# Optimization experiments

Hardware: AMD Instinct MI355X
Metric: run time of the kernel (lower is better)

## Reference

```python
import jax, jax.numpy as jnp
import numpy as np

N_SRC = 50000
N_DST = 50000
E = 1600000
IN_DIM = 128
OUT_DIM = 128
EDGE_DIM = 64
NUM_HEADS = 4
HEAD_DIM = OUT_DIM // NUM_HEADS


def setup_inputs() -> dict:
    key = jax.random.key(0)
    ks = jax.random.split(key, 10)
    return {
        "h_src": jax.random.normal(ks[0], (N_SRC, IN_DIM), dtype=jnp.float32),
        "h_dst": jax.random.normal(ks[1], (N_DST, IN_DIM), dtype=jnp.float32),
        "edge_feat": jax.random.normal(ks[2], (E, EDGE_DIM), dtype=jnp.float32),
        "edge_index": jnp.stack([
            jax.random.randint(ks[3], (E,), 0, N_SRC),
            jax.random.randint(ks[4], (E,), 0, N_DST),
        ], axis=0).astype(jnp.int64) if False else jnp.stack([
            jax.random.randint(ks[3], (E,), 0, N_SRC),
            jax.random.randint(ks[4], (E,), 0, N_DST),
        ], axis=0),
        # weights stored [in, out]; y = x @ W (same math as torch Linear with W^T)
        "W_src": jax.random.normal(ks[5], (IN_DIM, OUT_DIM), dtype=jnp.float32) * 0.05,
        "W_dst": jax.random.normal(ks[6], (IN_DIM, OUT_DIM), dtype=jnp.float32) * 0.05,
        "W_edge": jax.random.normal(ks[7], (EDGE_DIM, OUT_DIM), dtype=jnp.float32) * 0.05,
        "a_src": jax.random.normal(ks[8], (NUM_HEADS, HEAD_DIM), dtype=jnp.float32) * 0.1,
        "a_dst": jax.random.normal(ks[9], (NUM_HEADS, HEAD_DIM), dtype=jnp.float32) * 0.1,
        "a_edge": jax.random.normal(jax.random.fold_in(key, 10), (NUM_HEADS, HEAD_DIM), dtype=jnp.float32) * 0.1,
    }


def reference(h_src, h_dst, edge_feat, edge_index, W_src, W_dst, W_edge, a_src, a_dst, a_edge):
    num_dst = h_dst.shape[0]
    src_idx, dst_idx = edge_index[0], edge_index[1]

    hs = (h_src @ W_src).reshape(-1, NUM_HEADS, HEAD_DIM)   # [N_src, H, D]
    hd = (h_dst @ W_dst).reshape(-1, NUM_HEADS, HEAD_DIM)   # [N_dst, H, D]
    he = (edge_feat @ W_edge).reshape(-1, NUM_HEADS, HEAD_DIM)  # [E, H, D]

    # per-node attention logit components, gathered to edges
    e_src_n = jnp.einsum('nhd,hd->nh', hs, a_src)  # [N_src, H]
    e_dst_n = jnp.einsum('nhd,hd->nh', hd, a_dst)  # [N_dst, H]
    e_edge = jnp.einsum('ehd,hd->eh', he, a_edge)  # [E, H]
    e = e_src_n[src_idx] + e_dst_n[dst_idx] + e_edge  # [E, H]
    e = jnp.where(e > 0, e, 0.2 * e)  # leaky_relu(0.2)

    # segmented softmax over edges grouped by destination node
    e_max = jax.ops.segment_max(e, dst_idx, num_segments=num_dst)  # [N_dst, H]
    e_max = jnp.where(jnp.isfinite(e_max), e_max, 0.0)  # empty segments
    e_exp = jnp.exp(e - e_max[dst_idx])  # [E, H]
    e_sum = jax.ops.segment_sum(e_exp, dst_idx, num_segments=num_dst)  # [N_dst, H]
    alpha = e_exp / (e_sum[dst_idx] + 1e-8)  # [E, H]

    # weighted scatter-aggregate of source features
    msg = alpha[..., None] * hs[src_idx]  # [E, H, D]
    out = jax.ops.segment_sum(msg, dst_idx, num_segments=num_dst)  # [N_dst, H, D]
    return out.reshape(num_dst, NUM_HEADS * HEAD_DIM)
```

## Files before the change

### kernel.cpp

```cpp
#include <hip/hip_runtime.h>

typedef _Float16 half_t;

#define N_SRCN 50000
#define N_DSTN 50000
#define NE     1600000
#define IN_DIM 128
#define OUT_DIMN 128
#define EDGE_DIMN 64
#define NHEAD  4
#define HDIM   32

#define ROR_ADD(x, CTRL) ((x) + __int_as_float(__builtin_amdgcn_update_dpp( \
    0, __float_as_int(x), (CTRL), 0xF, 0xF, false)))
__device__ __forceinline__ float sum16(float s) {
    s = ROR_ADD(s, 0x121);
    s = ROR_ADD(s, 0x122);
    s = ROR_ADD(s, 0x124);
    s = ROR_ADD(s, 0x128);
    return s;
}


__global__ __launch_bounds__(512) void k_combine(
    const float* __restrict__ Wsrc, const float* __restrict__ Wdst,
    const float* __restrict__ Wedge,
    const float* __restrict__ asrc, const float* __restrict__ adst,
    const float* __restrict__ aedge,
    float* __restrict__ c_srcH, float* __restrict__ c_dstH,
    float* __restrict__ c_edgeH) {
    int t = threadIdx.x;
    int k = t >> 2, h = t & 3;
    float s1 = 0.f, s2 = 0.f;
    #pragma unroll
    for (int d = 0; d < HDIM; ++d) {
        s1 += Wsrc[k * OUT_DIMN + h * HDIM + d] * asrc[h * HDIM + d];
        s2 += Wdst[k * OUT_DIMN + h * HDIM + d] * adst[h * HDIM + d];
    }
    c_srcH[h * IN_DIM + k] = s1;
    c_dstH[h * IN_DIM + k] = s2;
    if (t < EDGE_DIMN * NHEAD) {
        float s3 = 0.f;
        #pragma unroll
        for (int d = 0; d < HDIM; ++d)
            s3 += Wedge[k * OUT_DIMN + h * HDIM + d] * aedge[h * HDIM + d];
        c_edgeH[h * EDGE_DIMN + k] = s3;
    }
}

__global__ __launch_bounds__(256) void k_node_logits(
    const float* __restrict__ X, const float* __restrict__ cH,
    float* __restrict__ outl, int N) {
    int t = threadIdx.x;
    int row = blockIdx.x * 16 + (t >> 4);
    int q = t & 15;
    if (row >= N) return;
    const float4* X4 = (const float4*)X;
    const float4* C4 = (const float4*)cH;
    float4 xa = X4[(size_t)row * 32 + q];
    float4 xb = X4[(size_t)row * 32 + 16 + q];
    float s0, s1, s2, s3;
    #pragma unroll
    for (int h = 0; h < 4; ++h) {
        float4 ca = C4[h * 32 + q];
        float4 cb = C4[h * 32 + 16 + q];
        float v = xa.x * ca.x + xa.y * ca.y + xa.z * ca.z + xa.w * ca.w
                + xb.x * cb.x + xb.y * cb.y + xb.z * cb.z + xb.w * cb.w;
        v = sum16(v);
        if (h == 0) s0 = v; else if (h == 1) s1 = v;
        else if (h == 2) s2 = v; else s3 = v;
    }
    float v = (q == 0) ? s0 : (q == 1) ? s1 : (q == 2) ? s2 : s3;
    if (q < 4) outl[(size_t)row * 4 + q] = v;
}

__global__ __launch_bounds__(256) void k_hist(
    const int* __restrict__ dstI, int* __restrict__ counts) {
    int e = blockIdx.x * 256 + threadIdx.x;
    if (e < NE) atomicAdd(&counts[dstI[e]], 1);
}

__global__ __launch_bounds__(1024) void k_scan_part(
    const int* __restrict__ cnt, int* __restrict__ offs, int* __restrict__ bsum) {
    __shared__ int wsum[16];
    int t = threadIdx.x, b = blockIdx.x;
    int idx = b * 1024 + t;
    int lane = t & 63, w = t >> 6;
    int c = (idx < N_DSTN) ? cnt[idx] : 0;
    int incl = c;
    #pragma unroll
    for (int off = 1; off < 64; off <<= 1) {
        int v = __shfl_up(incl, off, 64);
        if (lane >= off) incl += v;
    }
    if (lane == 63) wsum[w] = incl;
    __syncthreads();
    if (t == 0) {
        int run = 0;
        #pragma unroll
        for (int qq = 0; qq < 16; ++qq) { int v = wsum[qq]; wsum[qq] = run; run += v; }
        bsum[b] = run;
    }
    __syncthreads();
    if (idx < N_DSTN) offs[idx] = wsum[w] + incl - c;
}

__global__ __launch_bounds__(64) void k_scan_mid(
    int* __restrict__ bsum, int* __restrict__ offs, int nb) {
    int l = threadIdx.x;
    int v = (l < nb) ? bsum[l] : 0;
    int incl = v;
    #pragma unroll
    for (int off = 1; off < 64; off <<= 1) {
        int u = __shfl_up(incl, off, 64);
        if (l >= off) incl += u;
    }
    if (l < nb) bsum[l] = incl - v;
    if (l == 63) offs[N_DSTN] = incl;
}

__global__ __launch_bounds__(1024) void k_scan_add(
    int* __restrict__ offs, int* __restrict__ cursor, const int* __restrict__ bsum) {
    int idx = blockIdx.x * 1024 + threadIdx.x;
    if (idx < N_DSTN) {
        int v = offs[idx] + bsum[blockIdx.x];
        offs[idx] = v;
        cursor[idx] = v;
    }
}

__global__ __launch_bounds__(256) void k_scatter(
    const int* __restrict__ dstI, int* __restrict__ cursor,
    int* __restrict__ perm) {
    int e = blockIdx.x * 256 + threadIdx.x;
    if (e < NE) {
        int d = dstI[e];
        int pos = atomicAdd(&cursor[d], 1);
        perm[pos] = e;
    }
}

__global__ __launch_bounds__(256) void k_gemm_half(
    const float* __restrict__ A, const float* __restrict__ W,
    half_t* __restrict__ C, int M, int c0) {
    __shared__ float As[64][68];
    __shared__ float Ws[64][68];
    int t = threadIdx.x;
    int tx = t & 15, ty = t >> 4;
    int rowbase = blockIdx.x * 64;
    float acc[4][4];
    #pragma unroll
    for (int i = 0; i < 4; ++i)
        #pragma unroll
        for (int j = 0; j < 4; ++j) acc[i][j] = 0.f;

    for (int kc = 0; kc < IN_DIM; kc += 64) {
        #pragma unroll
        for (int p = 0; p < 4; ++p) {
            int flat = p * 1024 + t * 4;
            int r = flat >> 6, ck = flat & 63;
            float4 v = make_float4(0.f, 0.f, 0.f, 0.f);
            if (rowbase + r < M)
                v = *(const float4*)(A + (size_t)(rowbase + r) * IN_DIM + kc + ck);
            *(float4*)(&As[r][ck]) = v;
        }
        #pragma unroll
        for (int p = 0; p < 4; ++p) {
            int flat = p * 1024 + t * 4;
            int kk = flat >> 6, col = flat & 63;
            *(float4*)(&Ws[kk][col]) =
                *(const float4*)(W + (size_t)(kc + kk) * OUT_DIMN + c0 + col);
        }
        __syncthreads();
        #pragma unroll
        for (int k = 0; k < 64; ++k) {
            float a[4], b[4];
            #pragma unroll
            for (int i = 0; i < 4; ++i) a[i] = As[ty * 4 + i][k];
            #pragma unroll
            for (int j = 0; j < 4; ++j) b[j] = Ws[k][tx + j * 16];
            #pragma unroll
            for (int i = 0; i < 4; ++i)
                #pragma unroll
                for (int j = 0; j < 4; ++j) acc[i][j] += a[i] * b[j];
        }
        __syncthreads();
    }
    #pragma unroll
    for (int i = 0; i < 4; ++i) {
        int row = rowbase + ty * 4 + i;
        if (row < M) {
            #pragma unroll
            for (int j = 0; j < 4; ++j)
                C[(size_t)row * 64 + tx + j * 16] = (half_t)acc[i][j];
        }
    }
}

__global__ __launch_bounds__(256) void k_gather(
    const int* __restrict__ offs, const int* __restrict__ perm,
    const int* __restrict__ srcI,
    const float* __restrict__ EF, const float* __restrict__ ceH,
    const float* __restrict__ esrc, const float* __restrict__ edstl,
    const half_t* __restrict__ hsH, float* __restrict__ out, int pass) {
    int d = blockIdx.x * 4 + (threadIdx.x >> 6);
    if (d >= N_DSTN) return;
    int l = threadIdx.x & 63;
    int q = l & 15;
    int h = pass * 2 + (l >> 5);
    int start = offs[d], end = offs[d + 1];
    int n = end - start;
    if (n <= 0) { out[(size_t)d * OUT_DIMN + pass * 64 + l] = 0.f; return; }

    const float4* EF4 = (const float4*)EF;
    float4 c4 = ((const float4*)ceH)[h * 16 + q];
    float ed = edstl[(size_t)d * 4 + h];
    int end1 = end - 1;
    #define PCLAMP(i) perm[(start + (i) < end) ? (start + (i)) : end1]

    int a0 = PCLAMP(0), a1 = PCLAMP(1), a2 = PCLAMP(2);
    int e3 = PCLAMP(3), e4 = PCLAMP(4);
    int b0 = srcI[a0], b1 = srcI[a1], b2 = srcI[a2];
    int s3 = srcI[e3];
    float4 v0 = EF4[(size_t)a0 * 16 + q];
    float4 v1 = EF4[(size_t)a1 * 16 + q];
    float4 v2 = EF4[(size_t)a2 * 16 + q];
    float f0 = esrc[(size_t)b0 * 4 + h];
    float f1 = esrc[(size_t)b1 * 4 + h];
    float f2 = esrc[(size_t)b2 * 4 + h];
    half_t g0 = hsH[(size_t)b0 * 64 + l];
    half_t g1 = hsH[(size_t)b1 * 64 + l];
    half_t g2 = hsH[(size_t)b2 * 64 + l];

    float acc = 0.f, den = 0.f;
    for (int i = 0; i < n; ++i) {
        int e5 = PCLAMP(i + 5);
        int s4 = srcI[e4];
        float4 vN = EF4[(size_t)e3 * 16 + q];
        float  fN = esrc[(size_t)s3 * 4 + h];
        half_t gN = hsH[(size_t)s3 * 64 + l];

        float s = v0.x * c4.x + v0.y * c4.y + v0.z * c4.z + v0.w * c4.w;
        s = sum16(s);
        float z = f0 + ed + s;
        z = z > 0.f ? z : 0.2f * z;
        float ez = __expf(z);
        den += ez;
        acc += ez * (float)g0;

        v0 = v1; v1 = v2; v2 = vN;
        f0 = f1; f1 = f2; f2 = fN;
        g0 = g1; g1 = g2; g2 = gN;
        e3 = e4; e4 = e5; s3 = s4;
    }
    #undef PCLAMP
    out[(size_t)d * OUT_DIMN + pass * 64 + l] = acc / (den + 1e-8f);
}

extern "C" void kernel_launch(void* const* d_in, const int* in_sizes, int n_in,
                              void* d_out, int out_size, void* d_ws, size_t ws_size,
                              hipStream_t stream) {
    const float* h_src     = (const float*)d_in[0];
    const float* h_dst     = (const float*)d_in[1];
    const float* edge_feat = (const float*)d_in[2];
    const int*   eidx      = (const int*)d_in[3];
    const float* Wsrc      = (const float*)d_in[4];
    const float* Wdst      = (const float*)d_in[5];
    const float* Wedge     = (const float*)d_in[6];
    const float* asrc      = (const float*)d_in[7];
    const float* adst      = (const float*)d_in[8];
    const float* aedge     = (const float*)d_in[9];
    float* out = (float*)d_out;

    char* W = (char*)d_ws;
    half_t* hsH    = (half_t*)(W + 0);
    int*   perm    = (int*)(W + 6400000);
    float* esrc    = (float*)(W + 12800000);
    float* edstl   = (float*)(W + 13600000);
    int*   offs    = (int*)(W + 14400000);
    int*   cursor  = (int*)(W + 14600016);
    int*   counts  = (int*)(W + 14800016);
    float* c_srcH  = (float*)(W + 15000016);
    float* c_dstH  = (float*)(W + 15002064);
    float* c_edgeH = (float*)(W + 15004112);
    int*   bsum    = (int*)(W + 15005136);

    const int* srcI = eidx;
    const int* dstI = eidx + NE;

    const int NB_SCAN = (N_DSTN + 1023) / 1024;

    hipMemsetAsync(counts, 0, N_DSTN * sizeof(int), stream);

    k_combine<<<1, 512, 0, stream>>>(Wsrc, Wdst, Wedge, asrc, adst, aedge,
                                     c_srcH, c_dstH, c_edgeH);
    k_node_logits<<<(N_SRCN + 15) / 16, 256, 0, stream>>>(h_src, c_srcH, esrc, N_SRCN);
    k_node_logits<<<(N_DSTN + 15) / 16, 256, 0, stream>>>(h_dst, c_dstH, edstl, N_DSTN);

    k_hist<<<(NE + 255) / 256, 256, 0, stream>>>(dstI, counts);
    k_scan_part<<<NB_SCAN, 1024, 0, stream>>>(counts, offs, bsum);
    k_scan_mid<<<1, 64, 0, stream>>>(bsum, offs, NB_SCAN);
    k_scan_add<<<NB_SCAN, 1024, 0, stream>>>(offs, cursor, bsum);
    k_scatter<<<(NE + 255) / 256, 256, 0, stream>>>(dstI, cursor, perm);

    k_gemm_half<<<(N_SRCN + 63) / 64, 256, 0, stream>>>(h_src, Wsrc, hsH, N_SRCN, 0);
    k_gather<<<(N_DSTN + 3) / 4, 256, 0, stream>>>(offs, perm, srcI, edge_feat,
                                                   c_edgeH, esrc, edstl, hsH, out, 0);
    k_gemm_half<<<(N_SRCN + 63) / 64, 256, 0, stream>>>(h_src, Wsrc, hsH, N_SRCN, 64);
    k_gather<<<(N_DSTN + 3) / 4, 256, 0, stream>>>(offs, perm, srcI, edge_feat,
                                                   c_edgeH, esrc, edstl, hsH, out, 1);
}
```

Baseline: 1.405 ms.

## Stream edge logits in edge order and scatter compact CSR weights for gather

Edge-feature dot products and the exp'd leaky-relu logits are now computed in a coalesced pass over edges. That pass scatters 16-bit source indices and fp16 unnormalized weights into CSR order, replacing the perm-based random reads of 256-byte edge rows inside the gather. The gather now splits each head into four 32-column passes, with two half-waves each reducing half the edge list, and only reads compact per-edge arrays plus the source feature column. The cost is two edge-stream passes with atomics, four GEMM+gather passes instead of two, and fp16 storage of exp weights, which could overflow for large logits. It also relies on source ids fitting in 16 bits, which holds for 50000 nodes.

Result: faster. 1.216 ms (-13.4%).

```diff
diff --git a/kernel.cpp b/kernel.cpp
--- a/kernel.cpp
+++ b/kernel.cpp
@@ -120,37 +120,68 @@
 }
 
 __global__ __launch_bounds__(1024) void k_scan_add(
-    int* __restrict__ offs, int* __restrict__ cursor, const int* __restrict__ bsum) {
+    int* __restrict__ offs, int* __restrict__ curA, int* __restrict__ curB,
+    const int* __restrict__ bsum) {
     int idx = blockIdx.x * 1024 + threadIdx.x;
     if (idx < N_DSTN) {
         int v = offs[idx] + bsum[blockIdx.x];
         offs[idx] = v;
-        cursor[idx] = v;
-    }
-}
-
-__global__ __launch_bounds__(256) void k_scatter(
-    const int* __restrict__ dstI, int* __restrict__ cursor,
-    int* __restrict__ perm) {
-    int e = blockIdx.x * 256 + threadIdx.x;
-    if (e < NE) {
-        int d = dstI[e];
-        int pos = atomicAdd(&cursor[d], 1);
-        perm[pos] = e;
-    }
-}
-
-__global__ __launch_bounds__(256) void k_gemm_half(
+        curA[idx] = v;
+        curB[idx] = v;
+    }
+}
+
+__global__ __launch_bounds__(256) void k_edge_stream(
+    const float* __restrict__ EF,
+    const int* __restrict__ srcI, const int* __restrict__ dstI,
+    const float* __restrict__ esrc, const float* __restrict__ edstl,
+    const float* __restrict__ ceH, int* __restrict__ cursor,
+    unsigned short* __restrict__ ssrc,
+    half_t* __restrict__ wAo, half_t* __restrict__ wBo,
+    int ha, int hb) {
+    int t = threadIdx.x;
+    int e = blockIdx.x * 16 + (t >> 4);
+    if (e >= NE) return;
+    int q = t & 15;
+    const float4* EF4 = (const float4*)EF;
+    const float4* CE4 = (const float4*)ceH;
+    float4 v  = EF4[(size_t)e * 16 + q];
+    float4 cA = CE4[ha * 16 + q];
+    float4 cB = CE4[hb * 16 + q];
+    float sA = v.x * cA.x + v.y * cA.y + v.z * cA.z + v.w * cA.w;
+    float sB = v.x * cB.x + v.y * cB.y + v.z * cB.z + v.w * cB.w;
+    sA = sum16(sA);
+    sB = sum16(sB);
+    int pos = 0;
+    if (q < 2) {
+        int si = srcI[e], di = dstI[e];
+        int h = q ? hb : ha;
+        float s = q ? sB : sA;
+        float z = esrc[(size_t)si * 4 + h] + edstl[(size_t)di * 4 + h] + s;
+        z = z > 0.f ? z : 0.2f * z;
+        float ez = __expf(z);
+        if (q == 0) pos = atomicAdd(&cursor[di], 1);
+        pos = __shfl(pos, (t & 63) & ~15, 64);
+        if (q == 0) {
+            ssrc[pos] = (unsigned short)si;
+            wAo[pos] = (half_t)ez;
+        } else {
+            wBo[pos] = (half_t)ez;
+        }
+    }
+}
+
+__global__ __launch_bounds__(256) void k_gemm_q(
     const float* __restrict__ A, const float* __restrict__ W,
     half_t* __restrict__ C, int M, int c0) {
     __shared__ float As[64][68];
-    __shared__ float Ws[64][68];
+    __shared__ float Ws[64][36];
     int t = threadIdx.x;
-    int tx = t & 15, ty = t >> 4;
+    int tx = t & 7, ty = t >> 3;
     int rowbase = blockIdx.x * 64;
-    float acc[4][4];
-    #pragma unroll
-    for (int i = 0; i < 4; ++i)
+    float acc[2][4];
+    #pragma unroll
+    for (int i = 0; i < 2; ++i)
         #pragma unroll
         for (int j = 0; j < 4; ++j) acc[i][j] = 0.f;
 
@@ -165,96 +196,75 @@
             *(float4*)(&As[r][ck]) = v;
         }
         #pragma unroll
-        for (int p = 0; p < 4; ++p) {
+        for (int p = 0; p < 2; ++p) {
             int flat = p * 1024 + t * 4;
-            int kk = flat >> 6, col = flat & 63;
+            int kk = flat >> 5, col = flat & 31;
             *(float4*)(&Ws[kk][col]) =
                 *(const float4*)(W + (size_t)(kc + kk) * OUT_DIMN + c0 + col);
         }
         __syncthreads();
         #pragma unroll
         for (int k = 0; k < 64; ++k) {
-            float a[4], b[4];
+            float a[2], b[4];
             #pragma unroll
-            for (int i = 0; i < 4; ++i) a[i] = As[ty * 4 + i][k];
+            for (int i = 0; i < 2; ++i) a[i] = As[ty * 2 + i][k];
             #pragma unroll
-            for (int j = 0; j < 4; ++j) b[j] = Ws[k][tx + j * 16];
+            for (int j = 0; j < 4; ++j) b[j] = Ws[k][tx + j * 8];
             #pragma unroll
-            for (int i = 0; i < 4; ++i)
+            for (int i = 0; i < 2; ++i)
                 #pragma unroll
                 for (int j = 0; j < 4; ++j) acc[i][j] += a[i] * b[j];
         }
         __syncthreads();
     }
     #pragma unroll
-    for (int i = 0; i < 4; ++i) {
-        int row = rowbase + ty * 4 + i;
+    for (int i = 0; i < 2; ++i) {
+        int row = rowbase + ty * 2 + i;
         if (row < M) {
             #pragma unroll
             for (int j = 0; j < 4; ++j)
-                C[(size_t)row * 64 + tx + j * 16] = (half_t)acc[i][j];
+                C[(size_t)row * 32 + tx + j * 8] = (half_t)acc[i][j];
         }
     }
 }
 
 __global__ __launch_bounds__(256) void k_gather(
-    const int* __restrict__ offs, const int* __restrict__ perm,
-    const int* __restrict__ srcI,
-    const float* __restrict__ EF, const float* __restrict__ ceH,
-    const float* __restrict__ esrc, const float* __restrict__ edstl,
-    const half_t* __restrict__ hsH, float* __restrict__ out, int pass) {
+    const int* __restrict__ offs, const unsigned short* __restrict__ ssrc,
+    const half_t* __restrict__ wH, const half_t* __restrict__ hs_q,
+    float* __restrict__ out, int hcol) {
     int d = blockIdx.x * 4 + (threadIdx.x >> 6);
     if (d >= N_DSTN) return;
     int l = threadIdx.x & 63;
-    int q = l & 15;
-    int h = pass * 2 + (l >> 5);
+    int half = l >> 5, c = l & 31;
     int start = offs[d], end = offs[d + 1];
     int n = end - start;
-    if (n <= 0) { out[(size_t)d * OUT_DIMN + pass * 64 + l] = 0.f; return; }
-
-    const float4* EF4 = (const float4*)EF;
-    float4 c4 = ((const float4*)ceH)[h * 16 + q];
-    float ed = edstl[(size_t)d * 4 + h];
-    int end1 = end - 1;
-    #define PCLAMP(i) perm[(start + (i) < end) ? (start + (i)) : end1]
-
-    int a0 = PCLAMP(0), a1 = PCLAMP(1), a2 = PCLAMP(2);
-    int e3 = PCLAMP(3), e4 = PCLAMP(4);
-    int b0 = srcI[a0], b1 = srcI[a1], b2 = srcI[a2];
-    int s3 = srcI[e3];
-    float4 v0 = EF4[(size_t)a0 * 16 + q];
-    float4 v1 = EF4[(size_t)a1 * 16 + q];
-    float4 v2 = EF4[(size_t)a2 * 16 + q];
-    float f0 = esrc[(size_t)b0 * 4 + h];
-    float f1 = esrc[(size_t)b1 * 4 + h];
-    float f2 = esrc[(size_t)b2 * 4 + h];
-    half_t g0 = hsH[(size_t)b0 * 64 + l];
-    half_t g1 = hsH[(size_t)b1 * 64 + l];
-    half_t g2 = hsH[(size_t)b2 * 64 + l];
-
+    if (n <= 0) {
+        if (half == 0) out[(size_t)d * OUT_DIMN + hcol + c] = 0.f;
+        return;
+    }
+    int cntA = (n + 1) >> 1;
+    int myStart = start + (half ? cntA : 0);
+    int myN = half ? (n - cntA) : cntA;
+    int lim = (myN > 0) ? (myN - 1) : 0;
+    #define RIDX(j) (myStart + (((j) < lim) ? (j) : lim))
+
+    unsigned short s0 = ssrc[RIDX(0)], s1 = ssrc[RIDX(1)];
+    half_t w0 = wH[RIDX(0)], w1 = wH[RIDX(1)];
+    half_t h0 = hs_q[(size_t)s0 * 32 + c];
     float acc = 0.f, den = 0.f;
-    for (int i = 0; i < n; ++i) {
-        int e5 = PCLAMP(i + 5);
-        int s4 = srcI[e4];
-        float4 vN = EF4[(size_t)e3 * 16 + q];
-        float  fN = esrc[(size_t)s3 * 4 + h];
-        half_t gN = hsH[(size_t)s3 * 64 + l];
-
-        float s = v0.x * c4.x + v0.y * c4.y + v0.z * c4.z + v0.w * c4.w;
-        s = sum16(s);
-        float z = f0 + ed + s;
-        z = z > 0.f ? z : 0.2f * z;
-        float ez = __expf(z);
-        den += ez;
-        acc += ez * (float)g0;
-
-        v0 = v1; v1 = v2; v2 = vN;
-        f0 = f1; f1 = f2; f2 = fN;
-        g0 = g1; g1 = g2; g2 = gN;
-        e3 = e4; e4 = e5; s3 = s4;
-    }
-    #undef PCLAMP
-    out[(size_t)d * OUT_DIMN + pass * 64 + l] = acc / (den + 1e-8f);
+    for (int j = 0; j < cntA; ++j) {
+        unsigned short s2 = ssrc[RIDX(j + 2)];
+        half_t w2 = wH[RIDX(j + 2)];
+        half_t h1 = hs_q[(size_t)s1 * 32 + c];
+        float wf = (j < myN) ? (float)w0 : 0.f;
+        den += wf;
+        acc = fmaf(wf, (float)h0, acc);
+        s0 = s1; s1 = s2; w0 = w1; w1 = w2; h0 = h1;
+    }
+    #undef RIDX
+    acc += __shfl_xor(acc, 32, 64);
+    den += __shfl_xor(den, 32, 64);
+    if (half == 0) out[(size_t)d * OUT_DIMN + hcol + c] = acc / (den + 1e-8f);
 }
 
 extern "C" void kernel_launch(void* const* d_in, const int* in_sizes, int n_in,
@@ -273,17 +283,20 @@
     float* out = (float*)d_out;
 
     char* W = (char*)d_ws;
-    half_t* hsH    = (half_t*)(W + 0);
-    int*   perm    = (int*)(W + 6400000);
+    unsigned short* ssrc = (unsigned short*)(W + 0);
+    half_t* wA     = (half_t*)(W + 3200000);
+    half_t* wB     = (half_t*)(W + 6400000);
+    half_t* hs_q   = (half_t*)(W + 9600000);
     float* esrc    = (float*)(W + 12800000);
     float* edstl   = (float*)(W + 13600000);
     int*   offs    = (int*)(W + 14400000);
-    int*   cursor  = (int*)(W + 14600016);
-    int*   counts  = (int*)(W + 14800016);
-    float* c_srcH  = (float*)(W + 15000016);
-    float* c_dstH  = (float*)(W + 15002064);
-    float* c_edgeH = (float*)(W + 15004112);
-    int*   bsum    = (int*)(W + 15005136);
+    int*   curA    = (int*)(W + 14600016);
+    int*   curB    = (int*)(W + 14800016);
+    int*   counts  = (int*)(W + 15000016);
+    float* c_srcH  = (float*)(W + 15200016);
+    float* c_dstH  = (float*)(W + 15202064);
+    float* c_edgeH = (float*)(W + 15204112);
+    int*   bsum    = (int*)(W + 15205136);
 
     const int* srcI = eidx;
     const int* dstI = eidx + NE;
@@ -300,13 +313,19 @@
     k_hist<<<(NE + 255) / 256, 256, 0, stream>>>(dstI, counts);
     k_scan_part<<<NB_SCAN, 1024, 0, stream>>>(counts, offs, bsum);
     k_scan_mid<<<1, 64, 0, stream>>>(bsum, offs, NB_SCAN);
-    k_scan_add<<<NB_SCAN, 1024, 0, stream>>>(offs, cursor, bsum);
-    k_scatter<<<(NE + 255) / 256, 256, 0, stream>>>(dstI, cursor, perm);
-
-    k_gemm_half<<<(N_SRCN + 63) / 64, 256, 0, stream>>>(h_src, Wsrc, hsH, N_SRCN, 0);
-    k_gather<<<(N_DSTN + 3) / 4, 256, 0, stream>>>(offs, perm, srcI, edge_feat,
-                                                   c_edgeH, esrc, edstl, hsH, out, 0);
-    k_gemm_half<<<(N_SRCN + 63) / 64, 256, 0, stream>>>(h_src, Wsrc, hsH, N_SRCN, 64);
-    k_gather<<<(N_DSTN + 3) / 4, 256, 0, stream>>>(offs, perm, srcI, edge_feat,
-                                                   c_edgeH, esrc, edstl, hsH, out, 1);
-}
+    k_scan_add<<<NB_SCAN, 1024, 0, stream>>>(offs, curA, curB, bsum);
+
+    k_edge_stream<<<(NE + 15) / 16, 256, 0, stream>>>(
+        edge_feat, srcI, dstI, esrc, edstl, c_edgeH, curA, ssrc, wA, wB, 0, 1);
+    k_gemm_q<<<(N_SRCN + 63) / 64, 256, 0, stream>>>(h_src, Wsrc, hs_q, N_SRCN, 0);
+    k_gather<<<(N_DSTN + 3) / 4, 256, 0, stream>>>(offs, ssrc, wA, hs_q, out, 0);
+    k_gemm_q<<<(N_SRCN + 63) / 64, 256, 0, stream>>>(h_src, Wsrc, hs_q, N_SRCN, 32);
+    k_gather<<<(N_DSTN + 3) / 4, 256, 0, stream>>>(offs, ssrc, wB, hs_q, out, 32);
+
+    k_edge_stream<<<(NE + 15) / 16, 256, 0, stream>>>(
+        edge_feat, srcI, dstI, esrc, edstl, c_edgeH, curB, ssrc, wA, wB, 2, 3);
+    k_gemm_q<<<(N_SRCN + 63) / 64, 256, 0, stream>>>(h_src, Wsrc, hs_q, N_SRCN, 64);
+    k_gather<<<(N_DSTN + 3) / 4, 256, 0, stream>>>(offs, ssrc, wA, hs_q, out, 64);
+    k_gemm_q<<<(N_SRCN + 63) / 64, 256, 0, stream>>>(h_src, Wsrc, hs_q, N_SRCN, 96);
+    k_gather<<<(N_DSTN + 3) / 4, 256, 0, stream>>>(offs, ssrc, wB, hs_q, out, 96);
+}
```
